# Kernel tuning notes

Measured on AMD Instinct MI355X. Metric: run time of the kernel, lower is better.

The kernel has to match this reference:

```python
import jax, jax.numpy as jnp
import numpy as np

T, M, N = 16, 1024, 10000
N_IN, N_B = 8000, 100


def setup_inputs() -> dict:
    key = jax.random.key(0)
    ks = jax.random.split(key, 7)
    x = jax.random.normal(ks[0], (T, 3, M), dtype=jnp.float32)
    weight = jax.random.normal(ks[1], (N, 4 * M, 2), dtype=jnp.float32) * 0.02
    # 1-based node indices, as the original module subtracts 1
    node_in = jax.random.randint(ks[2], (N_IN,), 1, N + 1)
    top = jax.random.randint(ks[3], (N_B,), 1, N + 1)
    bottom = jax.random.randint(ks[4], (N_B,), 1, N + 1)
    left = jax.random.randint(ks[5], (N_B,), 1, N + 1)
    right = jax.random.randint(ks[6], (N_B,), 1, N + 1)
    return {"x": x, "weight": weight, "node_in": node_in,
            "top": top, "bottom": bottom, "left": left, "right": right}


def reference(x, weight, node_in, top, bottom, left, right):
    t, _, m = x.shape
    # Vectorized form of the nested scatter loop:
    # x_out[i, 4m:4m+4] = [x[i,0,m], x[i,2,m], x[i,2,m], x[i,1,m]]
    x_out = jnp.stack([x[:, 0, :], x[:, 2, :], x[:, 2, :], x[:, 1, :]],
                      axis=-1).reshape(t, 4 * m)  # [T, 4M]
    # torch.matmul([1,T,4M], [N,4M,2]) broadcast -> [N, T, 2]
    f = jnp.einsum('ti,nio->nto', x_out, weight)
    f_in = f[node_in - 1]  # [N_in, T, 2]
    s_top = f[top - 1, :, 1].sum(axis=0)      # [T]
    s_bot = f[bottom - 1, :, 1].sum(axis=0)
    s_left = f[left - 1, :, 0].sum(axis=0)
    s_right = f[right - 1, :, 0].sum(axis=0)
    f_b = jnp.stack([s_top, s_bot, s_left, s_right,
                     s_top + s_bot, s_left + s_right], axis=0)[..., None]  # [6, T, 1]
    return f_in, f_b
```

## Files before the change

### kernel.cpp

```cpp
#include <hip/hip_runtime.h>
#include <stdint.h>

#define T_DIM 16
#define M_DIM 1024
#define N_NODES 10000
#define NB 100
#define KI 4096
#define KP 8192
#define CHUNKS 8
#define I_CHUNK (KI / CHUNKS)
#define M_CHUNK (I_CHUNK / 4)
#define STEPS ((KP / CHUNKS) / 32)
#define PITCH (I_CHUNK + 4)
#define TILES 625
#define SLAB (N_NODES * T_DIM * 2)

typedef short short8 __attribute__((ext_vector_type(8)));
typedef float f32x4 __attribute__((ext_vector_type(4)));

__device__ __forceinline__ unsigned int fbits(float f) {
    return __builtin_bit_cast(unsigned int, f);
}
__device__ __forceinline__ unsigned int bf16rne(unsigned int u) {
    return (u + 0x7FFFu + ((u >> 16) & 1u)) >> 16;
}
__device__ __forceinline__ unsigned int pack2bf(float a, float b) {
    return bf16rne(fbits(a)) | (bf16rne(fbits(b)) << 16);
}

__global__ __launch_bounds__(256) void gemm_kernel(
    const float* __restrict__ x,
    const float* __restrict__ weight,
    float* __restrict__ fws)
{
    __shared__ unsigned short lds_x[T_DIM * PITCH];

    const int tid = threadIdx.x;
    const int chunk = blockIdx.y;

    for (int q = tid; q < T_DIM * M_CHUNK; q += 256) {
        int t = q >> 7;
        int mloc = q & 127;
        int m = chunk * M_CHUNK + mloc;
        const float* xb = x + t * 3 * M_DIM + m;
        float v0 = xb[0];
        float v1 = xb[M_DIM];
        float v2 = xb[2 * M_DIM];
        unsigned int w0 = pack2bf(v0, v2);
        unsigned int w1 = pack2bf(v2, v1);
        *(uint2*)&lds_x[t * PITCH + mloc * 4] = make_uint2(w0, w1);
    }
    __syncthreads();

    const int wave = tid >> 6;
    const int lane = tid & 63;
    const int tile = blockIdx.x * 4 + wave;
    if (tile >= TILES) return;

    const int col = lane & 15;
    const int quad = lane >> 4;
    const int n = tile * 16 + col;

    const float* wp =
        weight + (size_t)n * KP + (size_t)chunk * (KP / CHUNKS) + quad * 8;
    const unsigned short* xrow = &lds_x[(lane & 15) * PITCH + quad * 4];

    f32x4 acc0 = {0.f, 0.f, 0.f, 0.f};
    f32x4 acc1 = {0.f, 0.f, 0.f, 0.f};

    float4 flo = *(const float4*)wp;
    float4 fhi = *(const float4*)(wp + 4);
    #pragma unroll 4
    for (int s = 0; s < STEPS; ++s) {
        float4 lo = flo, hi = fhi;
        if (s + 1 < STEPS) {
            flo = *(const float4*)(wp + (s + 1) * 32);
            fhi = *(const float4*)(wp + (s + 1) * 32 + 4);
        }

        union { unsigned int ui[4]; short8 v; } B;
        B.ui[0] = pack2bf(lo.x, lo.y);
        B.ui[1] = pack2bf(lo.z, lo.w);
        B.ui[2] = pack2bf(hi.x, hi.y);
        B.ui[3] = pack2bf(hi.z, hi.w);

        uint2 u = *(const uint2*)(xrow + s * 16);
        union { unsigned int ui[4]; short8 v; } A0, A1;
        A0.ui[0] = u.x & 0xFFFFu;      A0.ui[1] = u.x >> 16;
        A0.ui[2] = u.y & 0xFFFFu;      A0.ui[3] = u.y >> 16;
        A1.ui[0] = u.x << 16;          A1.ui[1] = u.x & 0xFFFF0000u;
        A1.ui[2] = u.y << 16;          A1.ui[3] = u.y & 0xFFFF0000u;

        acc0 = __builtin_amdgcn_mfma_f32_16x16x32_bf16(A0.v, B.v, acc0, 0, 0, 0);
        acc1 = __builtin_amdgcn_mfma_f32_16x16x32_bf16(A1.v, B.v, acc1, 0, 0, 0);
    }

    float* slab = fws + (size_t)chunk * SLAB;
    #pragma unroll
    for (int r = 0; r < 4; ++r) {
        int t = quad * 4 + r;
        *(float2*)&slab[((size_t)n * T_DIM + t) * 2] = make_float2(acc0[r], acc1[r]);
    }
}

__global__ __launch_bounds__(256) void gather_kernel(
    const float* __restrict__ fws,
    const int* __restrict__ node_in,
    const int* __restrict__ top, const int* __restrict__ bottom,
    const int* __restrict__ left, const int* __restrict__ right,
    float* __restrict__ out)
{
    const int tid = threadIdx.x;
    if (blockIdx.x < 1000) {
        int e = blockIdx.x * 256 + tid;
        int j = e >> 5;
        int rem = e & 31;
        size_t base = (size_t)(node_in[j] - 1) * 32 + rem;
        float v = 0.f;
        #pragma unroll
        for (int c = 0; c < CHUNKS; ++c) v += fws[c * (size_t)SLAB + base];
        out[e] = v;
    } else {
        __shared__ float red[256];
        __shared__ float sums[64];
        const int l = tid >> 6;
        const int t = (tid >> 2) & 15;
        const int p = tid & 3;
        const int* lists[4] = {top, bottom, left, right};
        const int osel = (l < 2) ? 1 : 0;
        const int* lp = lists[l];
        float s = 0.f;
        for (int idx = p; idx < NB; idx += 4) {
            size_t base = (size_t)(lp[idx] - 1) * 32 + t * 2 + osel;
            #pragma unroll
            for (int c = 0; c < CHUNKS; ++c) s += fws[c * (size_t)SLAB + base];
        }
        red[tid] = s;
        __syncthreads();
        if (p == 0)
            sums[tid >> 2] = red[tid] + red[tid + 1] + red[tid + 2] + red[tid + 3];
        __syncthreads();
        if (tid < 96) {
            int row = tid >> 4;
            int tt = tid & 15;
            float v;
            if (row < 4)       v = sums[row * 16 + tt];
            else if (row == 4) v = sums[0 * 16 + tt] + sums[1 * 16 + tt];
            else               v = sums[2 * 16 + tt] + sums[3 * 16 + tt];
            out[256000 + tid] = v;
        }
    }
}

extern "C" void kernel_launch(void* const* d_in, const int* in_sizes, int n_in,
                              void* d_out, int out_size, void* d_ws, size_t ws_size,
                              hipStream_t stream)
{
    const float* x      = (const float*)d_in[0];
    const float* weight = (const float*)d_in[1];
    const int* node_in = (const int*)d_in[2];
    const int* top     = (const int*)d_in[3];
    const int* bottom  = (const int*)d_in[4];
    const int* left    = (const int*)d_in[5];
    const int* right   = (const int*)d_in[6];
    float* fws = (float*)d_ws;
    float* out = (float*)d_out;

    dim3 grid((TILES + 3) / 4, CHUNKS);
    gemm_kernel<<<grid, 256, 0, stream>>>(x, weight, fws);
    gather_kernel<<<1001, 256, 0, stream>>>(fws, node_in, top, bottom, left, right, out);
}
```

Before: 500.9 us.

## Compute GEMM only for nodes referenced by index lists via flag compaction

Adds two small kernels. One marks every node referenced by node_in or the boundary lists; the other compacts the marked nodes into a list with an atomic counter. The GEMM then walks only that compacted list, skipping the weight rows of nodes that are never read and cutting weight memory traffic. The flags are never cleared between calls, and the extra launches and the atomic compaction add a little fixed overhead.

```diff
diff --git a/kernel.cpp b/kernel.cpp
--- a/kernel.cpp
+++ b/kernel.cpp
@@ -5,6 +5,7 @@
 #define M_DIM 1024
 #define N_NODES 10000
 #define NB 100
+#define N_IN 8000
 #define KI 4096
 #define KP 8192
 #define CHUNKS 8
@@ -28,9 +29,40 @@
     return bf16rne(fbits(a)) | (bf16rne(fbits(b)) << 16);
 }
 
+__global__ __launch_bounds__(256) void flag_kernel(
+    const int* __restrict__ node_in,
+    const int* __restrict__ top, const int* __restrict__ bottom,
+    const int* __restrict__ left, const int* __restrict__ right,
+    int* __restrict__ flags, int* __restrict__ counter)
+{
+    int i = blockIdx.x * 256 + threadIdx.x;
+    if (i == 0) *counter = 0;
+    int v;
+    if (i < N_IN)               v = node_in[i];
+    else if (i < N_IN + NB)     v = top[i - N_IN];
+    else if (i < N_IN + 2*NB)   v = bottom[i - N_IN - NB];
+    else if (i < N_IN + 3*NB)   v = left[i - N_IN - 2*NB];
+    else if (i < N_IN + 4*NB)   v = right[i - N_IN - 3*NB];
+    else return;
+    flags[v - 1] = 1;
+}
+
+__global__ __launch_bounds__(256) void compact_kernel(
+    const int* __restrict__ flags, int* __restrict__ counter,
+    int* __restrict__ list)
+{
+    int i = blockIdx.x * 256 + threadIdx.x;
+    if (i < N_NODES && flags[i] == 1) {
+        int pos = atomicAdd(counter, 1);
+        list[pos] = i;
+    }
+}
+
 __global__ __launch_bounds__(256) void gemm_kernel(
     const float* __restrict__ x,
     const float* __restrict__ weight,
+    const int* __restrict__ list,
+    const int* __restrict__ counter,
     float* __restrict__ fws)
 {
     __shared__ unsigned short lds_x[T_DIM * PITCH];
@@ -52,14 +84,16 @@
     }
     __syncthreads();
 
+    const int cnt = *counter;
     const int wave = tid >> 6;
     const int lane = tid & 63;
     const int tile = blockIdx.x * 4 + wave;
-    if (tile >= TILES) return;
+    if (tile * 16 >= cnt) return;
 
     const int col = lane & 15;
     const int quad = lane >> 4;
-    const int n = tile * 16 + col;
+    const int idx = tile * 16 + col;
+    const int n = (idx < cnt) ? list[idx] : 0;
 
     const float* wp =
         weight + (size_t)n * KP + (size_t)chunk * (KP / CHUNKS) + quad * 8;
@@ -163,10 +197,18 @@
     const int* bottom  = (const int*)d_in[4];
     const int* left    = (const int*)d_in[5];
     const int* right   = (const int*)d_in[6];
-    float* fws = (float*)d_ws;
-    float* out = (float*)d_out;
+
+    float* fws   = (float*)d_ws;
+    int*   flags = (int*)(fws + (size_t)CHUNKS * SLAB);
+    int*   cnt   = flags + N_NODES;
+    int*   list  = cnt + 1;
+    float* out   = (float*)d_out;
+
+    flag_kernel<<<(N_IN + 4*NB + 255) / 256, 256, 0, stream>>>(
+        node_in, top, bottom, left, right, flags, cnt);
+    compact_kernel<<<(N_NODES + 255) / 256, 256, 0, stream>>>(flags, cnt, list);
 
     dim3 grid((TILES + 3) / 4, CHUNKS);
-    gemm_kernel<<<grid, 256, 0, stream>>>(x, weight, fws);
+    gemm_kernel<<<grid, 256, 0, stream>>>(x, weight, list, cnt, fws);
     gather_kernel<<<1001, 256, 0, stream>>>(fws, node_in, top, bottom, left, right, out);
 }
```

Measured after the change: 466.7 us. 6.8% less time.

## Compute GEMM only for nodes referenced by index lists; vectorize gather

Applied to the files above, without the earlier changes.

A new single-block kernel marks every node referenced by node_in and the four boundary lists, then compacts them into a list with a count. The GEMM then processes only those listed nodes, so it streams weight rows only for nodes whose outputs are actually used. This cuts the dominant weight traffic to roughly the unique referenced fraction, at the cost of an extra serial launch and a row order scattered across memory. The node_in gather is also widened to float4 loads and stores over 4x fewer blocks.

```diff
diff --git a/kernel.cpp b/kernel.cpp
--- a/kernel.cpp
+++ b/kernel.cpp
@@ -5,6 +5,7 @@
 #define M_DIM 1024
 #define N_NODES 10000
 #define NB 100
+#define N_IN 8000
 #define KI 4096
 #define KP 8192
 #define CHUNKS 8
@@ -28,9 +29,43 @@
     return bf16rne(fbits(a)) | (bf16rne(fbits(b)) << 16);
 }
 
+__global__ __launch_bounds__(1024) void dedup_kernel(
+    const int* __restrict__ node_in,
+    const int* __restrict__ top, const int* __restrict__ bottom,
+    const int* __restrict__ left, const int* __restrict__ right,
+    int* __restrict__ counter, int* __restrict__ list)
+{
+    __shared__ int flags[N_NODES];
+    __shared__ int lcnt;
+    const int tid = threadIdx.x;
+    for (int i = tid; i < N_NODES; i += 1024) flags[i] = 0;
+    if (tid == 0) lcnt = 0;
+    __syncthreads();
+    for (int i = tid; i < N_IN + 4 * NB; i += 1024) {
+        int v;
+        if (i < N_IN)              v = node_in[i];
+        else if (i < N_IN + NB)    v = top[i - N_IN];
+        else if (i < N_IN + 2*NB)  v = bottom[i - N_IN - NB];
+        else if (i < N_IN + 3*NB)  v = left[i - N_IN - 2*NB];
+        else                       v = right[i - N_IN - 3*NB];
+        flags[v - 1] = 1;
+    }
+    __syncthreads();
+    for (int i = tid; i < N_NODES; i += 1024) {
+        if (flags[i]) {
+            int pos = atomicAdd(&lcnt, 1);
+            list[pos] = i;
+        }
+    }
+    __syncthreads();
+    if (tid == 0) *counter = lcnt;
+}
+
 __global__ __launch_bounds__(256) void gemm_kernel(
     const float* __restrict__ x,
     const float* __restrict__ weight,
+    const int* __restrict__ list,
+    const int* __restrict__ counter,
     float* __restrict__ fws)
 {
     __shared__ unsigned short lds_x[T_DIM * PITCH];
@@ -52,14 +87,16 @@
     }
     __syncthreads();
 
+    const int cnt = *counter;
     const int wave = tid >> 6;
     const int lane = tid & 63;
     const int tile = blockIdx.x * 4 + wave;
-    if (tile >= TILES) return;
+    if (tile * 16 >= cnt) return;
 
     const int col = lane & 15;
     const int quad = lane >> 4;
-    const int n = tile * 16 + col;
+    const int idx = tile * 16 + col;
+    const int n = (idx < cnt) ? list[idx] : 0;
 
     const float* wp =
         weight + (size_t)n * KP + (size_t)chunk * (KP / CHUNKS) + quad * 8;
@@ -111,15 +148,18 @@
     float* __restrict__ out)
 {
     const int tid = threadIdx.x;
-    if (blockIdx.x < 1000) {
-        int e = blockIdx.x * 256 + tid;
-        int j = e >> 5;
-        int rem = e & 31;
+    if (blockIdx.x < 250) {
+        int e4 = blockIdx.x * 1024 + tid * 4;
+        int j = e4 >> 5;
+        int rem = e4 & 31;
         size_t base = (size_t)(node_in[j] - 1) * 32 + rem;
-        float v = 0.f;
+        float4 v = {0.f, 0.f, 0.f, 0.f};
         #pragma unroll
-        for (int c = 0; c < CHUNKS; ++c) v += fws[c * (size_t)SLAB + base];
-        out[e] = v;
+        for (int c = 0; c < CHUNKS; ++c) {
+            float4 s = *(const float4*)&fws[c * (size_t)SLAB + base];
+            v.x += s.x; v.y += s.y; v.z += s.z; v.w += s.w;
+        }
+        *(float4*)&out[e4] = v;
     } else {
         __shared__ float red[256];
         __shared__ float sums[64];
@@ -163,10 +203,15 @@
     const int* bottom  = (const int*)d_in[4];
     const int* left    = (const int*)d_in[5];
     const int* right   = (const int*)d_in[6];
-    float* fws = (float*)d_ws;
-    float* out = (float*)d_out;
+
+    float* fws  = (float*)d_ws;
+    int*   cnt  = (int*)(fws + (size_t)CHUNKS * SLAB);
+    int*   list = cnt + 1;
+    float* out  = (float*)d_out;
+
+    dedup_kernel<<<1, 1024, 0, stream>>>(node_in, top, bottom, left, right, cnt, list);
 
     dim3 grid((TILES + 3) / 4, CHUNKS);
-    gemm_kernel<<<grid, 256, 0, stream>>>(x, weight, fws);
-    gather_kernel<<<1001, 256, 0, stream>>>(fws, node_in, top, bottom, left, right, out);
-}
+    gemm_kernel<<<grid, 256, 0, stream>>>(x, weight, list, cnt, fws);
+    gather_kernel<<<251, 256, 0, stream>>>(fws, node_in, top, bottom, left, right, out);
+}
```

Result: faster. 465.9 us (-7.0%).
